# Kernel optimization log

Measured on AMD Instinct MI355X. Metric: run time of the kernel, lower is better.

The kernel has to match this reference:

```python
import jax, jax.numpy as jnp
import numpy as np

N, E, D = 40000, 320000, 128          # nodes, edges, model dim
H, C = 4, 128                          # GAT heads, per-head channels
DEPTH, MLP = 2, 512
NEG_SLOPE = 0.2
EPS_SM = 1e-16                         # PyG softmax denom epsilon


def layer_norm(x, g, b):
    mu = jnp.mean(x, axis=-1, keepdims=True)
    var = jnp.var(x, axis=-1, keepdims=True)
    return (x - mu) * jax.lax.rsqrt(var + 1e-5) * g + b


def gat_conv(x, src, dst, edge_attr, W, a_src, a_dst, We, a_edge, bias):
    # x: [N,D]; W: [D,H*C]; a_*: [H,C]; We: [1,H*C]; bias: [H*C]
    h = (x @ W).reshape(N, H, C)                       # [N,H,C]
    alpha_src = jnp.einsum('nhc,hc->nh', h, a_src)      # [N,H]
    alpha_dst = jnp.einsum('nhc,hc->nh', h, a_dst)      # [N,H]
    e = (edge_attr @ We).reshape(E, H, C)               # [E,H,C]
    alpha_e = jnp.einsum('ehc,hc->eh', e, a_edge)       # [E,H]
    alpha = alpha_src[src] + alpha_dst[dst] + alpha_e   # [E,H]
    alpha = jax.nn.leaky_relu(alpha, NEG_SLOPE)
    # segment softmax over edges sharing the same destination node
    amax = jax.ops.segment_max(alpha, dst, num_segments=N)   # [N,H]
    ex = jnp.exp(alpha - amax[dst])                          # [E,H]
    denom = jax.ops.segment_sum(ex, dst, num_segments=N)     # [N,H]
    attn = ex / (denom[dst] + EPS_SM)                        # [E,H]
    # message = attn * x_j ; aggregate by destination (scatter-add)
    msg = attn[:, :, None] * h[src]                          # [E,H,C]
    out = jax.ops.segment_sum(msg, dst, num_segments=N)      # [N,H,C]
    return out.reshape(N, H * C) + bias                      # concat heads


def setup_inputs():
    key = jax.random.key(0)
    ks = jax.random.split(key, 16)
    s = 0.05
    f32 = jnp.float32
    inp = {
        'x': jax.random.normal(ks[0], (N, D), f32),
        'edge_index': jax.random.randint(ks[1], (2, E), 0, N),
        'edge_attr': jax.random.normal(ks[2], (E, 1), f32),
        'ln1_g': jnp.ones((DEPTH, D), f32),
        'ln1_b': jnp.zeros((DEPTH, D), f32),
        'gat_W': jax.random.normal(ks[3], (DEPTH, D, H * C), f32) * s,
        'att_src': jax.random.normal(ks[4], (DEPTH, H, C), f32) * s,
        'att_dst': jax.random.normal(ks[5], (DEPTH, H, C), f32) * s,
        'edge_W': jax.random.normal(ks[6], (DEPTH, 1, H * C), f32) * s,
        'att_edge': jax.random.normal(ks[7], (DEPTH, H, C), f32) * s,
        'gat_bias': jnp.zeros((DEPTH, H * C), f32),
        'qf_W': jax.random.normal(ks[8], (DEPTH, H * C, D), f32) * s,
        'qf_b': jnp.zeros((DEPTH, D), f32),
        'ln2_g': jnp.ones((DEPTH, D), f32),
        'ln2_b': jnp.zeros((DEPTH, D), f32),
        'ff_W1': jax.random.normal(ks[9], (DEPTH, D, MLP), f32) * s,
        'ff_b1': jnp.zeros((DEPTH, MLP), f32),
        'ff_W2': jax.random.normal(ks[10], (DEPTH, MLP, D), f32) * s,
        'ff_b2': jnp.zeros((DEPTH, D), f32),
    }
    return inp


def reference(x, edge_index, edge_attr, ln1_g, ln1_b, gat_W, att_src, att_dst,
              edge_W, att_edge, gat_bias, qf_W, qf_b, ln2_g, ln2_b,
              ff_W1, ff_b1, ff_W2, ff_b2):
    src, dst = edge_index[0], edge_index[1]
    for d in range(DEPTH):
        # Residual(PreNorm(QuickFix(GATConv)))
        h = layer_norm(x, ln1_g[d], ln1_b[d])
        g = gat_conv(h, src, dst, edge_attr, gat_W[d], att_src[d], att_dst[d],
                     edge_W[d], att_edge[d], gat_bias[d])
        x = x + g @ qf_W[d] + qf_b[d]
        # Residual(PreNorm(FeedForward))
        h = layer_norm(x, ln2_g[d], ln2_b[d])
        x = x + jax.nn.gelu(h @ ff_W1[d] + ff_b1[d]) @ ff_W2[d] + ff_b2[d]
    return x
```

## Files before the change

kernel.cpp:

```cpp
#include <hip/hip_runtime.h>
#include <hip/hip_bf16.h>

#define N_NODES 40000
#define M_PAD   40064
#define N_EDGES 320000
#define DIM 128
#define HC 512
#define NHEAD 4
#define CHEAD 128
#define DEPTH_L 2
#define MLP_DIM 512
#define SCAN_NB ((N_NODES + 255) / 256)

typedef __attribute__((ext_vector_type(8))) short short8;
typedef __attribute__((ext_vector_type(4))) float f32x4;

static __device__ __forceinline__ void gload_lds16(const void* g, void* l)
{
    __builtin_amdgcn_global_load_lds(
        (const __attribute__((address_space(1))) unsigned int*)g,
        (__attribute__((address_space(3))) unsigned int*)l,
        16, 0, 0);
}

static __device__ __forceinline__ unsigned int packbf2(float a, float b)
{
    union { __hip_bfloat16 h[2]; unsigned int u; } p;
    p.h[0] = __float2bfloat16(a);
    p.h[1] = __float2bfloat16(b);
    return p.u;
}

static __device__ __forceinline__ float gelu_f(float v)
{
    float z2 = -1.5957691216f * (v + 0.044715f * v * v * v);
    return v / (1.f + __expf(z2));
}

__global__ __launch_bounds__(256) void k_ln(const float* __restrict__ x,
                                            const float* __restrict__ gma,
                                            const float* __restrict__ bta,
                                            __hip_bfloat16* __restrict__ out, int M)
{
    int row = blockIdx.x * 4 + (threadIdx.x >> 6);
    int lane = threadIdx.x & 63;
    if (row >= M) return;
    float2 v = *reinterpret_cast<const float2*>(x + (size_t)row * DIM + lane * 2);
    float s = v.x + v.y, sq = v.x * v.x + v.y * v.y;
    #pragma unroll
    for (int d = 32; d; d >>= 1) { s += __shfl_xor(s, d); sq += __shfl_xor(sq, d); }
    float mean = s * (1.f / DIM);
    float var = sq * (1.f / DIM) - mean * mean;
    float rs = rsqrtf(var + 1e-5f);
    int c = lane * 2;
    union { __hip_bfloat16 b[2]; unsigned int u; } p;
    p.b[0] = __float2bfloat16((v.x - mean) * rs * gma[c] + bta[c]);
    p.b[1] = __float2bfloat16((v.y - mean) * rs * gma[c + 1] + bta[c + 1]);
    *reinterpret_cast<unsigned int*>(out + (size_t)row * DIM + c) = p.u;
}

struct WcvtArgs {
    const float* src[4];
    __hip_bfloat16* dst[4];
    int K[4];
    int Nn[4];
};
__global__ __launch_bounds__(256) void k_wcvt4(WcvtArgs a)
{
    int j = blockIdx.y;
    int i = blockIdx.x * 256 + threadIdx.x;
    int K = a.K[j], N = a.Nn[j];
    if (i < K * N) {
        int n = i / K, k = i % K;
        a.dst[j][i] = __float2bfloat16(a.src[j][(size_t)k * N + n]);
    }
}

__global__ void k_prep_u(const float* __restrict__ gat_W,
                         const float* __restrict__ att_src,
                         const float* __restrict__ att_dst,
                         float* __restrict__ uvec)
{
    int b = blockIdx.x;
    int d = b >> 3, t8 = b & 7;
    int t = t8 >> 2, h = t8 & 3;
    int c = threadIdx.x;
    const float* W = gat_W + (size_t)d * DIM * HC;
    const float* av = (t == 0 ? att_src : att_dst) + (size_t)d * NHEAD * CHEAD + h * CHEAD;
    float s = 0.f;
    for (int cc = 0; cc < CHEAD; ++cc)
        s += W[(size_t)c * HC + h * CHEAD + cc] * av[cc];
    uvec[(size_t)d * 1024 + t8 * 128 + c] = s;
}

__global__ __launch_bounds__(256) void k_prep_m(const float* __restrict__ gat_W,
                                                const float* __restrict__ qf_W,
                                                __hip_bfloat16* __restrict__ Mt)
{
    int i = blockIdx.x * 256 + threadIdx.x;
    int d = i >> 16;
    int hk = (i >> 7) & 511;
    int j = i & 127;
    int h = hk >> 7, k = hk & 127;
    const float* W = gat_W + (size_t)d * DIM * HC + (size_t)k * HC + h * CHEAD;
    const float* Q = qf_W + (size_t)d * HC * DIM + (size_t)h * CHEAD * DIM + j;
    float s = 0.f;
    for (int c = 0; c < CHEAD; ++c)
        s += W[c] * Q[(size_t)c * DIM];
    Mt[(size_t)d * 65536 + (size_t)j * 512 + hk] = __float2bfloat16(s);
}

__global__ __launch_bounds__(256) void k_prep_c(const float* __restrict__ gat_bias,
                                                const float* __restrict__ qf_W,
                                                const float* __restrict__ qf_b,
                                                float* __restrict__ cvec)
{
    int idx = blockIdx.x * 4 + (threadIdx.x >> 6);
    int lane = threadIdx.x & 63;
    int d = idx >> 7, j = idx & 127;
    float s = 0.f;
    for (int m = lane; m < HC; m += 64)
        s += gat_bias[(size_t)d * HC + m] * qf_W[(size_t)d * HC * DIM + (size_t)m * DIM + j];
    #pragma unroll
    for (int dd = 32; dd; dd >>= 1) s += __shfl_xor(s, dd);
    if (lane == 0) cvec[idx] = s + qf_b[(size_t)d * DIM + j];
}

__global__ void k_ae(const float* __restrict__ We, const float* __restrict__ a_edge,
                     float* __restrict__ ae)
{
    int d = blockIdx.x;
    int h = threadIdx.x >> 6, lane = threadIdx.x & 63;
    float2 w = *reinterpret_cast<const float2*>(We + (size_t)d * HC + h * CHEAD + lane * 2);
    float2 a = *reinterpret_cast<const float2*>(a_edge + (size_t)d * NHEAD * CHEAD + h * CHEAD + lane * 2);
    float s = w.x * a.x + w.y * a.y;
    #pragma unroll
    for (int dd = 32; dd; dd >>= 1) s += __shfl_xor(s, dd);
    if (lane == 0) ae[d * 4 + h] = s;
}

__global__ __launch_bounds__(256) void k_dots(const unsigned int* __restrict__ hln,
                                              const float* __restrict__ uvec,
                                              float* __restrict__ asrc,
                                              float* __restrict__ adst)
{
    int n = blockIdx.x * 4 + (threadIdx.x >> 6);
    int lane = threadIdx.x & 63;
    unsigned int u = hln[n * 64 + lane];
    float f0 = __uint_as_float(u << 16);
    float f1 = __uint_as_float(u & 0xffff0000u);
    float s[8];
    #pragma unroll
    for (int t = 0; t < 8; ++t) {
        float2 uv = *reinterpret_cast<const float2*>(uvec + t * 128 + lane * 2);
        s[t] = f0 * uv.x + f1 * uv.y;
    }
    #pragma unroll
    for (int d = 32; d; d >>= 1) {
        #pragma unroll
        for (int t = 0; t < 8; ++t) s[t] += __shfl_xor(s[t], d);
    }
    if (lane == 0) {
        reinterpret_cast<float4*>(asrc)[n] = make_float4(s[0], s[1], s[2], s[3]);
        reinterpret_cast<float4*>(adst)[n] = make_float4(s[4], s[5], s[6], s[7]);
    }
}

__global__ __launch_bounds__(256) void k_alpha(const int* __restrict__ scsr,
                                               const int* __restrict__ dcsr,
                                               const float* __restrict__ eacsr,
                                               const float* __restrict__ asrc,
                                               const float* __restrict__ adst,
                                               const float* __restrict__ ae4v,
                                               float* __restrict__ wcsr)
{
    int p = blockIdx.x * 256 + threadIdx.x;
    if (p >= N_EDGES) return;
    int s = scsr[p], dd = dcsr[p];
    float q = eacsr[p];
    float4 as = reinterpret_cast<const float4*>(asrc)[s];
    float4 ad = reinterpret_cast<const float4*>(adst)[dd];
    float4 ae = *reinterpret_cast<const float4*>(ae4v);
    float4 w;
    float al;
    al = as.x + ad.x + ae.x * q; al = al > 0.f ? al : 0.2f * al; w.x = __expf(al);
    al = as.y + ad.y + ae.y * q; al = al > 0.f ? al : 0.2f * al; w.y = __expf(al);
    al = as.z + ad.z + ae.z * q; al = al > 0.f ? al : 0.2f * al; w.z = __expf(al);
    al = as.w + ad.w + ae.w * q; al = al > 0.f ? al : 0.2f * al; w.w = __expf(al);
    reinterpret_cast<float4*>(wcsr)[p] = w;
}

__global__ __launch_bounds__(256) void k_agg2(const int* __restrict__ off,
                                              const int* __restrict__ scsr,
                                              const float* __restrict__ wcsr,
                                              const unsigned int* __restrict__ hln,
                                              unsigned int* __restrict__ agg)
{
    int n = blockIdx.x * 4 + (threadIdx.x >> 6);
    int lane = threadIdx.x & 63;
    int e0 = off[n], e1 = off[n + 1];
    float den[4] = {0, 0, 0, 0};
    float accA[4] = {0, 0, 0, 0};
    float accB[4] = {0, 0, 0, 0};
    int i = e0;
    for (; i + 1 < e1; i += 2) {
        int s0 = scsr[i], s1 = scsr[i + 1];
        float4 w0 = reinterpret_cast<const float4*>(wcsr)[i];
        float4 w1 = reinterpret_cast<const float4*>(wcsr)[i + 1];
        unsigned int u0 = hln[s0 * 64 + lane];
        unsigned int u1 = hln[s1 * 64 + lane];
        float f00 = __uint_as_float(u0 << 16);
        float f01 = __uint_as_float(u0 & 0xffff0000u);
        float f10 = __uint_as_float(u1 << 16);
        float f11 = __uint_as_float(u1 & 0xffff0000u);
        den[0] += w0.x + w1.x; den[1] += w0.y + w1.y;
        den[2] += w0.z + w1.z; den[3] += w0.w + w1.w;
        accA[0] += w0.x * f00 + w1.x * f10; accB[0] += w0.x * f01 + w1.x * f11;
        accA[1] += w0.y * f00 + w1.y * f10; accB[1] += w0.y * f01 + w1.y * f11;
        accA[2] += w0.z * f00 + w1.z * f10; accB[2] += w0.z * f01 + w1.z * f11;
        accA[3] += w0.w * f00 + w1.w * f10; accB[3] += w0.w * f01 + w1.w * f11;
    }
    if (i < e1) {
        int s0 = scsr[i];
        float4 w0 = reinterpret_cast<const float4*>(wcsr)[i];
        unsigned int u0 = hln[s0 * 64 + lane];
        float f00 = __uint_as_float(u0 << 16);
        float f01 = __uint_as_float(u0 & 0xffff0000u);
        den[0] += w0.x; den[1] += w0.y; den[2] += w0.z; den[3] += w0.w;
        accA[0] += w0.x * f00; accB[0] += w0.x * f01;
        accA[1] += w0.y * f00; accB[1] += w0.y * f01;
        accA[2] += w0.z * f00; accB[2] += w0.z * f01;
        accA[3] += w0.w * f00; accB[3] += w0.w * f01;
    }
    #pragma unroll
    for (int h = 0; h < 4; ++h) {
        float inv = 1.f / (den[h] + 1e-16f);
        agg[n * 256 + h * 64 + lane] = packbf2(accA[h] * inv, accB[h] * inv);
    }
}

template <bool LN>
__global__ __launch_bounds__(256) void k_qf(const short* __restrict__ A,
                                            const short* __restrict__ Bt,
                                            const float* __restrict__ bias,
                                            const float* __restrict__ resid,
                                            float* __restrict__ xout,
                                            const float* __restrict__ gma,
                                            const float* __restrict__ bta,
                                            __hip_bfloat16* __restrict__ hout,
                                            int M)
{
    __shared__ __align__(16) short Bls[2][128 * 64];
    const int tid = threadIdx.x;
    const int lane = tid & 63;
    const int w = tid >> 6;
    const int lrow = lane & 15;
    const int lk = lane >> 4;
    const int mw = blockIdx.x * 64 + w * 16;

    auto stage = [&](int buf, int kt) {
        #pragma unroll
        for (int c0 = 0; c0 < 1024; c0 += 256) {
            int c = c0 + tid;
            int wb = c0 + (w << 6);
            int r = c >> 3, gq = c & 7, gp = gq ^ (r & 7);
            gload_lds16(Bt + (size_t)r * 512 + kt + gp * 8, &Bls[buf][wb * 8]);
        }
    };

    f32x4 acc[8] = {};
    stage(0, 0);
    __syncthreads();
    int cur = 0;
    for (int t = 0; t < 8; ++t) {
        if (t < 7) stage(cur ^ 1, (t + 1) * 64);
        #pragma unroll
        for (int ks = 0; ks < 2; ++ks) {
            short8 af = *reinterpret_cast<const short8*>(
                A + (size_t)(mw + lrow) * 512 + t * 64 + ks * 32 + lk * 8);
            short8 bf[8];
            #pragma unroll
            for (int fj = 0; fj < 8; ++fj) {
                int r = fj * 16 + lrow;
                int g = ks * 4 + lk;
                bf[fj] = *reinterpret_cast<const short8*>(
                    &Bls[cur][r * 64 + ((g ^ (r & 7)) * 8)]);
            }
            #pragma unroll
            for (int fj = 0; fj < 8; ++fj)
                acc[fj] = __builtin_amdgcn_mfma_f32_16x16x32_bf16(
                    af, bf[fj], acc[fj], 0, 0, 0);
        }
        __syncthreads();
        cur ^= 1;
    }

    #pragma unroll
    for (int p = 0; p < 4; ++p) {
        int m = mw + lk * 4 + p;
        float v[8], s = 0.f, sq = 0.f;
        #pragma unroll
        for (int fj = 0; fj < 8; ++fj) {
            int n = fj * 16 + lrow;
            v[fj] = acc[fj][p] + bias[n] + resid[(size_t)m * DIM + n];
            s += v[fj]; sq += v[fj] * v[fj];
        }
        #pragma unroll
        for (int fj = 0; fj < 8; ++fj)
            xout[(size_t)m * DIM + fj * 16 + lrow] = v[fj];
        if (LN) {
            #pragma unroll
            for (int d = 1; d < 16; d <<= 1) {
                s += __shfl_xor(s, d);
                sq += __shfl_xor(sq, d);
            }
            float mean = s * (1.f / DIM);
            float var = sq * (1.f / DIM) - mean * mean;
            float rs = rsqrtf(var + 1e-5f);
            #pragma unroll
            for (int fj = 0; fj < 8; ++fj) {
                int n = fj * 16 + lrow;
                hout[(size_t)m * DIM + n] =
                    __float2bfloat16((v[fj] - mean) * rs * gma[n] + bta[n]);
            }
        }
    }
}

template <bool LN>
__global__ __launch_bounds__(256) void k_ff(const short* __restrict__ A,
                                            const short* __restrict__ W1t,
                                            const short* __restrict__ W2t,
                                            const float* __restrict__ b1,
                                            const float* __restrict__ b2,
                                            const float* __restrict__ resid,
                                            float* __restrict__ xout,
                                            const float* __restrict__ gma,
                                            const float* __restrict__ bta,
                                            __hip_bfloat16* __restrict__ hout,
                                            int M)
{
    __shared__ __align__(16) short B1ls[64 * 128];
    __shared__ __align__(16) short B2ls[128 * 64];
    __shared__ __align__(16) short midls[4][16 * 64];
    const int tid = threadIdx.x;
    const int lane = tid & 63;
    const int w = tid >> 6;
    const int lrow = lane & 15;
    const int lk = lane >> 4;
    const int mw = blockIdx.x * 64 + w * 16;
    __hip_bfloat16* midw = (__hip_bfloat16*)midls[w];

    short8 af[4];
    #pragma unroll
    for (int ks = 0; ks < 4; ++ks)
        af[ks] = *reinterpret_cast<const short8*>(
            A + (size_t)(mw + lrow) * 128 + ks * 32 + lk * 8);

    auto stage1 = [&](int mc) {
        #pragma unroll
        for (int c0 = 0; c0 < 1024; c0 += 256) {
            int c = c0 + tid;
            int wb = c0 + (w << 6);
            int r = c >> 4, gq = c & 15, gp = gq ^ (r & 15);
            gload_lds16(W1t + (size_t)(mc * 64 + r) * 128 + gp * 8, &B1ls[wb * 8]);
        }
    };
    auto stage2 = [&](int mc) {
        #pragma unroll
        for (int c0 = 0; c0 < 1024; c0 += 256) {
            int c = c0 + tid;
            int wb = c0 + (w << 6);
            int r = c >> 3, gq = c & 7, gp = gq ^ (r & 7);
            gload_lds16(W2t + (size_t)r * 512 + mc * 64 + gp * 8, &B2ls[wb * 8]);
        }
    };

    f32x4 acc2[8] = {};
    stage1(0);
    for (int mc = 0; mc < 8; ++mc) {
        __syncthreads();
        stage2(mc);
        f32x4 acc1[4] = {};
        #pragma unroll
        for (int ks = 0; ks < 4; ++ks) {
            short8 bf1[4];
            #pragma unroll
            for (int fj = 0; fj < 4; ++fj) {
                int r = fj * 16 + lrow;
                bf1[fj] = *reinterpret_cast<const short8*>(
                    &B1ls[r * 128 + (((ks * 4 + lk) ^ (r & 15)) * 8)]);
            }
            #pragma unroll
            for (int fj = 0; fj < 4; ++fj)
                acc1[fj] = __builtin_amdgcn_mfma_f32_16x16x32_bf16(
                    af[ks], bf1[fj], acc1[fj], 0, 0, 0);
        }
        #pragma unroll
        for (int fj = 0; fj < 4; ++fj) {
            #pragma unroll
            for (int p = 0; p < 4; ++p) {
                int mloc = lk * 4 + p;
                int cloc = fj * 16 + lrow;
                float v = gelu_f(acc1[fj][p] + b1[mc * 64 + cloc]);
                int slot = (cloc >> 3) ^ (mloc & 7);
                midw[mloc * 64 + slot * 8 + (cloc & 7)] = __float2bfloat16(v);
            }
        }
        __syncthreads();
        if (mc < 7) stage1(mc + 1);
        #pragma unroll
        for (int ks2 = 0; ks2 < 2; ++ks2) {
            int g = ks2 * 4 + lk;
            short8 a2 = *reinterpret_cast<const short8*>(
                &midls[w][lrow * 64 + ((g ^ (lrow & 7)) * 8)]);
            short8 bf2[8];
            #pragma unroll
            for (int fj = 0; fj < 8; ++fj) {
                int r = fj * 16 + lrow;
                bf2[fj] = *reinterpret_cast<const short8*>(
                    &B2ls[r * 64 + (((g ^ (r & 7))) * 8)]);
            }
            #pragma unroll
            for (int fj = 0; fj < 8; ++fj)
                acc2[fj] = __builtin_amdgcn_mfma_f32_16x16x32_bf16(
                    a2, bf2[fj], acc2[fj], 0, 0, 0);
        }
    }

    #pragma unroll
    for (int p = 0; p < 4; ++p) {
        int m = mw + lk * 4 + p;
        float v[8], s = 0.f, sq = 0.f;
        #pragma unroll
        for (int fj = 0; fj < 8; ++fj) {
            int n = fj * 16 + lrow;
            v[fj] = acc2[fj][p] + b2[n] + resid[(size_t)m * DIM + n];
            s += v[fj]; sq += v[fj] * v[fj];
        }
        #pragma unroll
        for (int fj = 0; fj < 8; ++fj)
            xout[(size_t)m * DIM + fj * 16 + lrow] = v[fj];
        if (LN) {
            #pragma unroll
            for (int d = 1; d < 16; d <<= 1) {
                s += __shfl_xor(s, d);
                sq += __shfl_xor(sq, d);
            }
            float mean = s * (1.f / DIM);
            float var = sq * (1.f / DIM) - mean * mean;
            float rs = rsqrtf(var + 1e-5f);
            #pragma unroll
            for (int fj = 0; fj < 8; ++fj) {
                int n = fj * 16 + lrow;
                hout[(size_t)m * DIM + n] =
                    __float2bfloat16((v[fj] - mean) * rs * gma[n] + bta[n]);
            }
        }
    }
}

__global__ void k_hist(const int* __restrict__ dst, int* __restrict__ deg)
{
    int e = blockIdx.x * 256 + threadIdx.x;
    if (e < N_EDGES) atomicAdd(&deg[dst[e]], 1);
}

__global__ __launch_bounds__(256) void k_scan1(const int* __restrict__ deg,
                                               int* __restrict__ off,
                                               int* __restrict__ bsum)
{
    __shared__ int wsum[4];
    int b = blockIdx.x;
    int t = threadIdx.x, lane = t & 63, w = t >> 6;
    int i = b * 256 + t;
    int v = (i < N_NODES) ? deg[i] : 0;
    int s = v;
    #pragma unroll
    for (int d = 1; d < 64; d <<= 1) {
        int u = __shfl_up(s, d);
        if (lane >= d) s += u;
    }
    if (lane == 63) wsum[w] = s;
    __syncthreads();
    int wpre = 0;
    #pragma unroll
    for (int j = 0; j < 4; ++j)
        if (j < w) wpre += wsum[j];
    if (i < N_NODES) off[i] = wpre + s - v;
    if (t == 255) bsum[b] = wpre + s;
}

__global__ __launch_bounds__(256) void k_scan2(int* __restrict__ bsum,
                                               int* __restrict__ bpre)
{
    __shared__ int wsum[4];
    int t = threadIdx.x, lane = t & 63, w = t >> 6;
    int v = (t < SCAN_NB) ? bsum[t] : 0;
    int s = v;
    #pragma unroll
    for (int d = 1; d < 64; d <<= 1) {
        int u = __shfl_up(s, d);
        if (lane >= d) s += u;
    }
    if (lane == 63) wsum[w] = s;
    __syncthreads();
    int wpre = 0;
    #pragma unroll
    for (int j = 0; j < 4; ++j)
        if (j < w) wpre += wsum[j];
    if (t < SCAN_NB) bpre[t] = wpre + s - v;
    if (t == 255) bpre[SCAN_NB] = wpre + s;
}

__global__ __launch_bounds__(256) void k_scan3(int* __restrict__ off,
                                               const int* __restrict__ bpre,
                                               int* __restrict__ cur)
{
    int b = blockIdx.x;
    int i = b * 256 + threadIdx.x;
    if (i < N_NODES) {
        int o = off[i] + bpre[b];
        off[i] = o;
        cur[i] = o;
    }
    if (i == 0) off[N_NODES] = bpre[SCAN_NB];
}

__global__ void k_fill(const int* __restrict__ src, const int* __restrict__ dst,
                       const float* __restrict__ ea, int* __restrict__ cur,
                       int* __restrict__ scsr, int* __restrict__ dcsr,
                       float* __restrict__ eacsr)
{
    int e = blockIdx.x * 256 + threadIdx.x;
    if (e < N_EDGES) {
        int dd = dst[e];
        int p = atomicAdd(&cur[dd], 1);
        scsr[p] = src[e];
        dcsr[p] = dd;
        eacsr[p] = ea[e];
    }
}

extern "C" void kernel_launch(void* const* d_in, const int* in_sizes, int n_in,
                              void* d_out, int out_size, void* d_ws, size_t ws_size,
                              hipStream_t stream)
{
    const float* x_in     = (const float*)d_in[0];
    const int*   ei       = (const int*)d_in[1];
    const float* ea       = (const float*)d_in[2];
    const float* ln1_g    = (const float*)d_in[3];
    const float* ln1_b    = (const float*)d_in[4];
    const float* gat_W    = (const float*)d_in[5];
    const float* att_src  = (const float*)d_in[6];
    const float* att_dst  = (const float*)d_in[7];
    const float* edge_W   = (const float*)d_in[8];
    const float* att_edge = (const float*)d_in[9];
    const float* gat_bias = (const float*)d_in[10];
    const float* qf_W     = (const float*)d_in[11];
    const float* qf_b     = (const float*)d_in[12];
    const float* ln2_g    = (const float*)d_in[13];
    const float* ln2_b    = (const float*)d_in[14];
    const float* ff_W1    = (const float*)d_in[15];
    const float* ff_b1    = (const float*)d_in[16];
    const float* ff_W2    = (const float*)d_in[17];
    const float* ff_b2    = (const float*)d_in[18];
    float* x = (float*)d_out;

    char* ws = (char*)d_ws;
    size_t o = 0;
    auto alloc = [&](size_t b) { size_t r = o; o += (b + 255) & ~(size_t)255; return r; };
    __hip_bfloat16*  h_ln  = (__hip_bfloat16*)(ws + alloc((size_t)M_PAD * DIM * 2));
    __hip_bfloat16*  gbuf  = (__hip_bfloat16*)(ws + alloc((size_t)M_PAD * HC * 2));
    float*           asrc  = (float*)(ws + alloc((size_t)N_NODES * 4 * 4));
    float*           adst  = (float*)(ws + alloc((size_t)N_NODES * 4 * 4));
    float*           ae4   = (float*)(ws + alloc(256));
    float*           uvec  = (float*)(ws + alloc((size_t)DEPTH_L * 1024 * 4));
    __hip_bfloat16*  Mt    = (__hip_bfloat16*)(ws + alloc((size_t)DEPTH_L * 65536 * 2));
    float*           cvec  = (float*)(ws + alloc(256 * 4));
    int*             deg   = (int*)(ws + alloc((size_t)(N_NODES + 1) * 4));
    int*             off   = (int*)(ws + alloc((size_t)(N_NODES + 1) * 4));
    int*             cur   = (int*)(ws + alloc((size_t)N_NODES * 4));
    int*             bsum  = (int*)(ws + alloc((size_t)(SCAN_NB + 1) * 4));
    int*             bpre  = (int*)(ws + alloc((size_t)(SCAN_NB + 1) * 4));
    int*             scsr  = (int*)(ws + alloc((size_t)N_EDGES * 4));
    int*             dcsr  = (int*)(ws + alloc((size_t)N_EDGES * 4));
    float*           eacsr = (float*)(ws + alloc((size_t)N_EDGES * 4));
    float*           wcsr  = (float*)(ws + alloc((size_t)N_EDGES * 4 * 4));
    __hip_bfloat16* Wt[DEPTH_L][2];
    for (int d = 0; d < DEPTH_L; ++d)
        for (int j = 0; j < 2; ++j)
            Wt[d][j] = (__hip_bfloat16*)(ws + alloc((size_t)65536 * 2));

    const int* srcA = ei;
    const int* dstA = ei + N_EDGES;

    WcvtArgs wa;
    for (int d = 0; d < DEPTH_L; ++d) {
        wa.src[d * 2 + 0] = ff_W1 + (size_t)d * DIM * MLP_DIM; wa.K[d * 2 + 0] = DIM;     wa.Nn[d * 2 + 0] = MLP_DIM;
        wa.src[d * 2 + 1] = ff_W2 + (size_t)d * MLP_DIM * DIM; wa.K[d * 2 + 1] = MLP_DIM; wa.Nn[d * 2 + 1] = DIM;
        wa.dst[d * 2 + 0] = Wt[d][0];
        wa.dst[d * 2 + 1] = Wt[d][1];
    }
    k_wcvt4<<<dim3(256, 4), 256, 0, stream>>>(wa);
    k_prep_u<<<16, 128, 0, stream>>>(gat_W, att_src, att_dst, uvec);
    k_prep_m<<<512, 256, 0, stream>>>(gat_W, qf_W, Mt);
    k_prep_c<<<64, 256, 0, stream>>>(gat_bias, qf_W, qf_b, cvec);
    k_ae<<<2, 256, 0, stream>>>(edge_W, att_edge, ae4);

    hipMemsetAsync(deg, 0, (size_t)(N_NODES + 1) * 4, stream);
    k_hist<<<(N_EDGES + 255) / 256, 256, 0, stream>>>(dstA, deg);
    k_scan1<<<SCAN_NB, 256, 0, stream>>>(deg, off, bsum);
    k_scan2<<<1, 256, 0, stream>>>(bsum, bpre);
    k_scan3<<<SCAN_NB, 256, 0, stream>>>(off, bpre, cur);
    k_fill<<<(N_EDGES + 255) / 256, 256, 0, stream>>>(srcA, dstA, ea, cur, scsr, dcsr, eacsr);

    const int QB = N_NODES / 64;
    const int NB = N_NODES / 4;
    const int EB = (N_EDGES + 255) / 256;

    k_ln<<<NB, 256, 0, stream>>>(x_in, ln1_g, ln1_b, h_ln, N_NODES);
    k_dots<<<NB, 256, 0, stream>>>((const unsigned int*)h_ln, uvec, asrc, adst);

    for (int d = 0; d < DEPTH_L; ++d) {
        const float* resid0 = (d == 0) ? x_in : x;
        k_alpha<<<EB, 256, 0, stream>>>(scsr, dcsr, eacsr, asrc, adst, ae4 + d * 4, wcsr);
        k_agg2<<<NB, 256, 0, stream>>>(off, scsr, wcsr, (const unsigned int*)h_ln,
            (unsigned int*)gbuf);
        k_qf<true><<<QB, 256, 0, stream>>>((const short*)gbuf,
            (const short*)(Mt + (size_t)d * 65536), cvec + d * 128, resid0, x,
            ln2_g + d * DIM, ln2_b + d * DIM, h_ln, N_NODES);
        if (d + 1 < DEPTH_L) {
            k_ff<true><<<QB, 256, 0, stream>>>((const short*)h_ln,
                (const short*)Wt[d][0], (const short*)Wt[d][1],
                ff_b1 + d * MLP_DIM, ff_b2 + d * DIM, x, x,
                ln1_g + (d + 1) * DIM, ln1_b + (d + 1) * DIM, h_ln, N_NODES);
            k_dots<<<NB, 256, 0, stream>>>((const unsigned int*)h_ln,
                uvec + (size_t)(d + 1) * 1024, asrc, adst);
        } else {
            k_ff<false><<<QB, 256, 0, stream>>>((const short*)h_ln,
                (const short*)Wt[d][0], (const short*)Wt[d][1],
                ff_b1 + d * MLP_DIM, ff_b2 + d * DIM, x, x,
                nullptr, nullptr, nullptr, N_NODES);
        }
    }
}
```

Measured before the change: 295.9 us.

## Merge prep kernels, build CSR in one grid-barrier kernel, fuse LN with dots

Folds the five weight-preprocessing kernels into one block-indexed k_prep launch. Replaces the memset, histogram, three scan kernels and fill with a single persistent k_csr kernel that separates its phases with atomic-counter grid barriers. Fuses the first LayerNorm with the attention-score dot products, and preloads all A fragments into registers in k_qf. The goal is fewer launches and less intermediate traffic; the cost is reliance on all 512 CSR blocks being co-resident for the spin barrier, plus higher register pressure in k_qf.

```diff
diff --git a/kernel.cpp b/kernel.cpp
--- a/kernel.cpp
+++ b/kernel.cpp
@@ -2,7 +2,6 @@
 #include <hip/hip_bf16.h>
 
 #define N_NODES 40000
-#define M_PAD   40064
 #define N_EDGES 320000
 #define DIM 128
 #define HC 512
@@ -11,6 +10,7 @@
 #define DEPTH_L 2
 #define MLP_DIM 512
 #define SCAN_NB ((N_NODES + 255) / 256)
+#define CSR_NB 512
 
 typedef __attribute__((ext_vector_type(8))) short short8;
 typedef __attribute__((ext_vector_type(4))) float f32x4;
@@ -37,10 +37,185 @@
     return v / (1.f + __expf(z2));
 }
 
+struct PrepArgs {
+    const float* wsrc[4];
+    __hip_bfloat16* wdst[4];
+    int wK[4];
+    int wN[4];
+    const float* gat_W;
+    const float* att_src;
+    const float* att_dst;
+    const float* edge_W;
+    const float* att_edge;
+    const float* gat_bias;
+    const float* qf_W;
+    const float* qf_b;
+    float* uvec;
+    __hip_bfloat16* Mt;
+    float* cvec;
+    float* ae;
+    int* cnt;
+};
+__global__ __launch_bounds__(256) void k_prep(PrepArgs a)
+{
+    int b = blockIdx.x;
+    int tid = threadIdx.x;
+    if (b < 1024) {
+        int j = b >> 8;
+        int i = (b & 255) * 256 + tid;
+        int K = a.wK[j], N = a.wN[j];
+        if (i < K * N) {
+            int n = i / K, k = i % K;
+            a.wdst[j][i] = __float2bfloat16(a.wsrc[j][(size_t)k * N + n]);
+        }
+    } else if (b < 1040) {
+        if (tid < 128) {
+            int bb = b - 1024;
+            int d = bb >> 3, t8 = bb & 7;
+            int t = t8 >> 2, h = t8 & 3;
+            int c = tid;
+            const float* W = a.gat_W + (size_t)d * DIM * HC;
+            const float* av = (t == 0 ? a.att_src : a.att_dst)
+                              + (size_t)d * NHEAD * CHEAD + h * CHEAD;
+            float s = 0.f;
+            for (int cc = 0; cc < CHEAD; ++cc)
+                s += W[(size_t)c * HC + h * CHEAD + cc] * av[cc];
+            a.uvec[(size_t)d * 1024 + t8 * 128 + c] = s;
+        }
+    } else if (b < 1552) {
+        int i = (b - 1040) * 256 + tid;
+        int d = i >> 16;
+        int hk = (i >> 7) & 511;
+        int j = i & 127;
+        int h = hk >> 7, k = hk & 127;
+        const float* W = a.gat_W + (size_t)d * DIM * HC + (size_t)k * HC + h * CHEAD;
+        const float* Q = a.qf_W + (size_t)d * HC * DIM + (size_t)h * CHEAD * DIM + j;
+        float s = 0.f;
+        for (int c = 0; c < CHEAD; ++c)
+            s += W[c] * Q[(size_t)c * DIM];
+        a.Mt[(size_t)d * 65536 + (size_t)j * 512 + hk] = __float2bfloat16(s);
+    } else if (b < 1616) {
+        int idx = (b - 1552) * 4 + (tid >> 6);
+        int lane = tid & 63;
+        int d = idx >> 7, j = idx & 127;
+        float s = 0.f;
+        for (int m = lane; m < HC; m += 64)
+            s += a.gat_bias[(size_t)d * HC + m]
+               * a.qf_W[(size_t)d * HC * DIM + (size_t)m * DIM + j];
+        #pragma unroll
+        for (int dd = 32; dd; dd >>= 1) s += __shfl_xor(s, dd);
+        if (lane == 0) a.cvec[idx] = s + a.qf_b[(size_t)d * DIM + j];
+    } else if (b < 1618) {
+        int d = b - 1616;
+        int h = tid >> 6, lane = tid & 63;
+        float2 w = *reinterpret_cast<const float2*>(
+            a.edge_W + (size_t)d * HC + h * CHEAD + lane * 2);
+        float2 av = *reinterpret_cast<const float2*>(
+            a.att_edge + (size_t)d * NHEAD * CHEAD + h * CHEAD + lane * 2);
+        float s = w.x * av.x + w.y * av.y;
+        #pragma unroll
+        for (int dd = 32; dd; dd >>= 1) s += __shfl_xor(s, dd);
+        if (lane == 0) a.ae[d * 4 + h] = s;
+    } else {
+        if (tid < 8) a.cnt[tid] = 0;
+    }
+}
+
+static __device__ __forceinline__ void gbar(int* cnt, int phase)
+{
+    __syncthreads();
+    if (threadIdx.x == 0) {
+        __threadfence();
+        atomicAdd(&cnt[phase], 1);
+        while (atomicAdd(&cnt[phase], 0) < CSR_NB) __builtin_amdgcn_s_sleep(8);
+        __threadfence();
+    }
+    __syncthreads();
+}
+
+__global__ __launch_bounds__(256) void k_csr(const int* __restrict__ src,
+                                             const int* __restrict__ dst,
+                                             const float* __restrict__ ea,
+                                             int* __restrict__ deg,
+                                             int* __restrict__ off,
+                                             int* __restrict__ cur,
+                                             int* __restrict__ bsum,
+                                             int* __restrict__ bpre,
+                                             int* __restrict__ scsr,
+                                             int* __restrict__ dcsr,
+                                             float* __restrict__ eacsr,
+                                             int* cnt)
+{
+    __shared__ int wsum[4];
+    int t = threadIdx.x, lane = t & 63, w = t >> 6;
+    int gtid = blockIdx.x * 256 + t;
+    const int gsz = CSR_NB * 256;
+
+    for (int i = gtid; i <= N_NODES; i += gsz) deg[i] = 0;
+    gbar(cnt, 0);
+    for (int e = gtid; e < N_EDGES; e += gsz) atomicAdd(&deg[dst[e]], 1);
+    gbar(cnt, 1);
+    for (int b = blockIdx.x; b < SCAN_NB; b += CSR_NB) {
+        int i = b * 256 + t;
+        int v = (i < N_NODES) ? deg[i] : 0;
+        int s = v;
+        #pragma unroll
+        for (int d = 1; d < 64; d <<= 1) {
+            int u = __shfl_up(s, d);
+            if (lane >= d) s += u;
+        }
+        if (lane == 63) wsum[w] = s;
+        __syncthreads();
+        int wpre = 0;
+        #pragma unroll
+        for (int j = 0; j < 4; ++j)
+            if (j < w) wpre += wsum[j];
+        if (i < N_NODES) off[i] = wpre + s - v;
+        if (t == 255) bsum[b] = wpre + s;
+        __syncthreads();
+    }
+    gbar(cnt, 2);
+    if (blockIdx.x == 0) {
+        int v = (t < SCAN_NB) ? bsum[t] : 0;
+        int s = v;
+        #pragma unroll
+        for (int d = 1; d < 64; d <<= 1) {
+            int u = __shfl_up(s, d);
+            if (lane >= d) s += u;
+        }
+        if (lane == 63) wsum[w] = s;
+        __syncthreads();
+        int wpre = 0;
+        #pragma unroll
+        for (int j = 0; j < 4; ++j)
+            if (j < w) wpre += wsum[j];
+        if (t < SCAN_NB) bpre[t] = wpre + s - v;
+        if (t == 255) bpre[SCAN_NB] = wpre + s;
+    }
+    gbar(cnt, 3);
+    for (int i = gtid; i < N_NODES; i += gsz) {
+        int o = off[i] + bpre[i >> 8];
+        off[i] = o;
+        cur[i] = o;
+    }
+    if (gtid == 0) off[N_NODES] = bpre[SCAN_NB];
+    gbar(cnt, 4);
+    for (int e = gtid; e < N_EDGES; e += gsz) {
+        int dd = dst[e];
+        int p = atomicAdd(&cur[dd], 1);
+        scsr[p] = src[e];
+        dcsr[p] = dd;
+        eacsr[p] = ea[e];
+    }
+}
+
 __global__ __launch_bounds__(256) void k_ln(const float* __restrict__ x,
                                             const float* __restrict__ gma,
                                             const float* __restrict__ bta,
-                                            __hip_bfloat16* __restrict__ out, int M)
+                                            const float* __restrict__ uvec,
+                                            __hip_bfloat16* __restrict__ out,
+                                            float* __restrict__ asrc,
+                                            float* __restrict__ adst, int M)
 {
     int row = blockIdx.x * 4 + (threadIdx.x >> 6);
     int lane = threadIdx.x & 63;
@@ -53,90 +228,24 @@
     float var = sq * (1.f / DIM) - mean * mean;
     float rs = rsqrtf(var + 1e-5f);
     int c = lane * 2;
-    union { __hip_bfloat16 b[2]; unsigned int u; } p;
-    p.b[0] = __float2bfloat16((v.x - mean) * rs * gma[c] + bta[c]);
-    p.b[1] = __float2bfloat16((v.y - mean) * rs * gma[c + 1] + bta[c + 1]);
-    *reinterpret_cast<unsigned int*>(out + (size_t)row * DIM + c) = p.u;
-}
-
-struct WcvtArgs {
-    const float* src[4];
-    __hip_bfloat16* dst[4];
-    int K[4];
-    int Nn[4];
-};
-__global__ __launch_bounds__(256) void k_wcvt4(WcvtArgs a)
-{
-    int j = blockIdx.y;
-    int i = blockIdx.x * 256 + threadIdx.x;
-    int K = a.K[j], N = a.Nn[j];
-    if (i < K * N) {
-        int n = i / K, k = i % K;
-        a.dst[j][i] = __float2bfloat16(a.src[j][(size_t)k * N + n]);
-    }
-}
-
-__global__ void k_prep_u(const float* __restrict__ gat_W,
-                         const float* __restrict__ att_src,
-                         const float* __restrict__ att_dst,
-                         float* __restrict__ uvec)
-{
-    int b = blockIdx.x;
-    int d = b >> 3, t8 = b & 7;
-    int t = t8 >> 2, h = t8 & 3;
-    int c = threadIdx.x;
-    const float* W = gat_W + (size_t)d * DIM * HC;
-    const float* av = (t == 0 ? att_src : att_dst) + (size_t)d * NHEAD * CHEAD + h * CHEAD;
-    float s = 0.f;
-    for (int cc = 0; cc < CHEAD; ++cc)
-        s += W[(size_t)c * HC + h * CHEAD + cc] * av[cc];
-    uvec[(size_t)d * 1024 + t8 * 128 + c] = s;
-}
-
-__global__ __launch_bounds__(256) void k_prep_m(const float* __restrict__ gat_W,
-                                                const float* __restrict__ qf_W,
-                                                __hip_bfloat16* __restrict__ Mt)
-{
-    int i = blockIdx.x * 256 + threadIdx.x;
-    int d = i >> 16;
-    int hk = (i >> 7) & 511;
-    int j = i & 127;
-    int h = hk >> 7, k = hk & 127;
-    const float* W = gat_W + (size_t)d * DIM * HC + (size_t)k * HC + h * CHEAD;
-    const float* Q = qf_W + (size_t)d * HC * DIM + (size_t)h * CHEAD * DIM + j;
-    float s = 0.f;
-    for (int c = 0; c < CHEAD; ++c)
-        s += W[c] * Q[(size_t)c * DIM];
-    Mt[(size_t)d * 65536 + (size_t)j * 512 + hk] = __float2bfloat16(s);
-}
-
-__global__ __launch_bounds__(256) void k_prep_c(const float* __restrict__ gat_bias,
-                                                const float* __restrict__ qf_W,
-                                                const float* __restrict__ qf_b,
-                                                float* __restrict__ cvec)
-{
-    int idx = blockIdx.x * 4 + (threadIdx.x >> 6);
-    int lane = threadIdx.x & 63;
-    int d = idx >> 7, j = idx & 127;
-    float s = 0.f;
-    for (int m = lane; m < HC; m += 64)
-        s += gat_bias[(size_t)d * HC + m] * qf_W[(size_t)d * HC * DIM + (size_t)m * DIM + j];
-    #pragma unroll
-    for (int dd = 32; dd; dd >>= 1) s += __shfl_xor(s, dd);
-    if (lane == 0) cvec[idx] = s + qf_b[(size_t)d * DIM + j];
-}
-
-__global__ void k_ae(const float* __restrict__ We, const float* __restrict__ a_edge,
-                     float* __restrict__ ae)
-{
-    int d = blockIdx.x;
-    int h = threadIdx.x >> 6, lane = threadIdx.x & 63;
-    float2 w = *reinterpret_cast<const float2*>(We + (size_t)d * HC + h * CHEAD + lane * 2);
-    float2 a = *reinterpret_cast<const float2*>(a_edge + (size_t)d * NHEAD * CHEAD + h * CHEAD + lane * 2);
-    float s = w.x * a.x + w.y * a.y;
-    #pragma unroll
-    for (int dd = 32; dd; dd >>= 1) s += __shfl_xor(s, dd);
-    if (lane == 0) ae[d * 4 + h] = s;
+    float h0 = (v.x - mean) * rs * gma[c] + bta[c];
+    float h1 = (v.y - mean) * rs * gma[c + 1] + bta[c + 1];
+    *reinterpret_cast<unsigned int*>(out + (size_t)row * DIM + c) = packbf2(h0, h1);
+    float ss[8];
+    #pragma unroll
+    for (int tt = 0; tt < 8; ++tt) {
+        float2 uv = *reinterpret_cast<const float2*>(uvec + tt * 128 + c);
+        ss[tt] = h0 * uv.x + h1 * uv.y;
+    }
+    #pragma unroll
+    for (int d = 32; d; d >>= 1) {
+        #pragma unroll
+        for (int tt = 0; tt < 8; ++tt) ss[tt] += __shfl_xor(ss[tt], d);
+    }
+    if (lane == 0) {
+        reinterpret_cast<float4*>(asrc)[row] = make_float4(ss[0], ss[1], ss[2], ss[3]);
+        reinterpret_cast<float4*>(adst)[row] = make_float4(ss[4], ss[5], ss[6], ss[7]);
+    }
 }
 
 __global__ __launch_bounds__(256) void k_dots(const unsigned int* __restrict__ hln,
@@ -258,6 +367,12 @@
     const int lk = lane >> 4;
     const int mw = blockIdx.x * 64 + w * 16;
 
+    short8 aq[16];
+    #pragma unroll
+    for (int t = 0; t < 16; ++t)
+        aq[t] = *reinterpret_cast<const short8*>(
+            A + (size_t)(mw + lrow) * 512 + t * 32 + lk * 8);
+
     auto stage = [&](int buf, int kt) {
         #pragma unroll
         for (int c0 = 0; c0 < 1024; c0 += 256) {
@@ -276,8 +391,7 @@
         if (t < 7) stage(cur ^ 1, (t + 1) * 64);
         #pragma unroll
         for (int ks = 0; ks < 2; ++ks) {
-            short8 af = *reinterpret_cast<const short8*>(
-                A + (size_t)(mw + lrow) * 512 + t * 64 + ks * 32 + lk * 8);
+            short8 af = aq[t * 2 + ks];
             short8 bf[8];
             #pragma unroll
             for (int fj = 0; fj < 8; ++fj) {
@@ -327,7 +441,7 @@
     }
 }
 
-template <bool LN>
+template <bool LNN>
 __global__ __launch_bounds__(256) void k_ff(const short* __restrict__ A,
                                             const short* __restrict__ W1t,
                                             const short* __restrict__ W2t,
@@ -419,7 +533,7 @@
             for (int fj = 0; fj < 8; ++fj) {
                 int r = fj * 16 + lrow;
                 bf2[fj] = *reinterpret_cast<const short8*>(
-                    &B2ls[r * 64 + (((g ^ (r & 7))) * 8)]);
+                    &B2ls[r * 64 + ((g ^ (r & 7)) * 8)]);
             }
             #pragma unroll
             for (int fj = 0; fj < 8; ++fj)
@@ -441,7 +555,7 @@
         #pragma unroll
         for (int fj = 0; fj < 8; ++fj)
             xout[(size_t)m * DIM + fj * 16 + lrow] = v[fj];
-        if (LN) {
+        if (LNN) {
             #pragma unroll
             for (int d = 1; d < 16; d <<= 1) {
                 s += __shfl_xor(s, d);
@@ -457,88 +571,6 @@
                     __float2bfloat16((v[fj] - mean) * rs * gma[n] + bta[n]);
             }
         }
-    }
-}
-
-__global__ void k_hist(const int* __restrict__ dst, int* __restrict__ deg)
-{
-    int e = blockIdx.x * 256 + threadIdx.x;
-    if (e < N_EDGES) atomicAdd(&deg[dst[e]], 1);
-}
-
-__global__ __launch_bounds__(256) void k_scan1(const int* __restrict__ deg,
-                                               int* __restrict__ off,
-                                               int* __restrict__ bsum)
-{
-    __shared__ int wsum[4];
-    int b = blockIdx.x;
-    int t = threadIdx.x, lane = t & 63, w = t >> 6;
-    int i = b * 256 + t;
-    int v = (i < N_NODES) ? deg[i] : 0;
-    int s = v;
-    #pragma unroll
-    for (int d = 1; d < 64; d <<= 1) {
-        int u = __shfl_up(s, d);
-        if (lane >= d) s += u;
-    }
-    if (lane == 63) wsum[w] = s;
-    __syncthreads();
-    int wpre = 0;
-    #pragma unroll
-    for (int j = 0; j < 4; ++j)
-        if (j < w) wpre += wsum[j];
-    if (i < N_NODES) off[i] = wpre + s - v;
-    if (t == 255) bsum[b] = wpre + s;
-}
-
-__global__ __launch_bounds__(256) void k_scan2(int* __restrict__ bsum,
-                                               int* __restrict__ bpre)
-{
-    __shared__ int wsum[4];
-    int t = threadIdx.x, lane = t & 63, w = t >> 6;
-    int v = (t < SCAN_NB) ? bsum[t] : 0;
-    int s = v;
-    #pragma unroll
-    for (int d = 1; d < 64; d <<= 1) {
-        int u = __shfl_up(s, d);
-        if (lane >= d) s += u;
-    }
-    if (lane == 63) wsum[w] = s;
-    __syncthreads();
-    int wpre = 0;
-    #pragma unroll
-    for (int j = 0; j < 4; ++j)
-        if (j < w) wpre += wsum[j];
-    if (t < SCAN_NB) bpre[t] = wpre + s - v;
-    if (t == 255) bpre[SCAN_NB] = wpre + s;
-}
-
-__global__ __launch_bounds__(256) void k_scan3(int* __restrict__ off,
-                                               const int* __restrict__ bpre,
-                                               int* __restrict__ cur)
-{
-    int b = blockIdx.x;
-    int i = b * 256 + threadIdx.x;
-    if (i < N_NODES) {
-        int o = off[i] + bpre[b];
-        off[i] = o;
-        cur[i] = o;
-    }
-    if (i == 0) off[N_NODES] = bpre[SCAN_NB];
-}
-
-__global__ void k_fill(const int* __restrict__ src, const int* __restrict__ dst,
-                       const float* __restrict__ ea, int* __restrict__ cur,
-                       int* __restrict__ scsr, int* __restrict__ dcsr,
-                       float* __restrict__ eacsr)
-{
-    int e = blockIdx.x * 256 + threadIdx.x;
-    if (e < N_EDGES) {
-        int dd = dst[e];
-        int p = atomicAdd(&cur[dd], 1);
-        scsr[p] = src[e];
-        dcsr[p] = dd;
-        eacsr[p] = ea[e];
     }
 }
 
@@ -570,14 +602,15 @@
     char* ws = (char*)d_ws;
     size_t o = 0;
     auto alloc = [&](size_t b) { size_t r = o; o += (b + 255) & ~(size_t)255; return r; };
-    __hip_bfloat16*  h_ln  = (__hip_bfloat16*)(ws + alloc((size_t)M_PAD * DIM * 2));
-    __hip_bfloat16*  gbuf  = (__hip_bfloat16*)(ws + alloc((size_t)M_PAD * HC * 2));
+    __hip_bfloat16*  h_ln  = (__hip_bfloat16*)(ws + alloc((size_t)N_NODES * DIM * 2));
+    __hip_bfloat16*  gbuf  = (__hip_bfloat16*)(ws + alloc((size_t)N_NODES * HC * 2));
     float*           asrc  = (float*)(ws + alloc((size_t)N_NODES * 4 * 4));
     float*           adst  = (float*)(ws + alloc((size_t)N_NODES * 4 * 4));
     float*           ae4   = (float*)(ws + alloc(256));
     float*           uvec  = (float*)(ws + alloc((size_t)DEPTH_L * 1024 * 4));
     __hip_bfloat16*  Mt    = (__hip_bfloat16*)(ws + alloc((size_t)DEPTH_L * 65536 * 2));
     float*           cvec  = (float*)(ws + alloc(256 * 4));
+    int*             cnt   = (int*)(ws + alloc(64));
     int*             deg   = (int*)(ws + alloc((size_t)(N_NODES + 1) * 4));
     int*             off   = (int*)(ws + alloc((size_t)(N_NODES + 1) * 4));
     int*             cur   = (int*)(ws + alloc((size_t)N_NODES * 4));
@@ -595,32 +628,29 @@
     const int* srcA = ei;
     const int* dstA = ei + N_EDGES;
 
-    WcvtArgs wa;
+    PrepArgs pa;
     for (int d = 0; d < DEPTH_L; ++d) {
-        wa.src[d * 2 + 0] = ff_W1 + (size_t)d * DIM * MLP_DIM; wa.K[d * 2 + 0] = DIM;     wa.Nn[d * 2 + 0] = MLP_DIM;
-        wa.src[d * 2 + 1] = ff_W2 + (size_t)d * MLP_DIM * DIM; wa.K[d * 2 + 1] = MLP_DIM; wa.Nn[d * 2 + 1] = DIM;
-        wa.dst[d * 2 + 0] = Wt[d][0];
-        wa.dst[d * 2 + 1] = Wt[d][1];
-    }
-    k_wcvt4<<<dim3(256, 4), 256, 0, stream>>>(wa);
-    k_prep_u<<<16, 128, 0, stream>>>(gat_W, att_src, att_dst, uvec);
-    k_prep_m<<<512, 256, 0, stream>>>(gat_W, qf_W, Mt);
-    k_prep_c<<<64, 256, 0, stream>>>(gat_bias, qf_W, qf_b, cvec);
-    k_ae<<<2, 256, 0, stream>>>(edge_W, att_edge, ae4);
-
-    hipMemsetAsync(deg, 0, (size_t)(N_NODES + 1) * 4, stream);
-    k_hist<<<(N_EDGES + 255) / 256, 256, 0, stream>>>(dstA, deg);
-    k_scan1<<<SCAN_NB, 256, 0, stream>>>(deg, off, bsum);
-    k_scan2<<<1, 256, 0, stream>>>(bsum, bpre);
-    k_scan3<<<SCAN_NB, 256, 0, stream>>>(off, bpre, cur);
-    k_fill<<<(N_EDGES + 255) / 256, 256, 0, stream>>>(srcA, dstA, ea, cur, scsr, dcsr, eacsr);
+        pa.wsrc[d * 2 + 0] = ff_W1 + (size_t)d * DIM * MLP_DIM;
+        pa.wK[d * 2 + 0] = DIM;     pa.wN[d * 2 + 0] = MLP_DIM;
+        pa.wsrc[d * 2 + 1] = ff_W2 + (size_t)d * MLP_DIM * DIM;
+        pa.wK[d * 2 + 1] = MLP_DIM; pa.wN[d * 2 + 1] = DIM;
+        pa.wdst[d * 2 + 0] = Wt[d][0];
+        pa.wdst[d * 2 + 1] = Wt[d][1];
+    }
+    pa.gat_W = gat_W; pa.att_src = att_src; pa.att_dst = att_dst;
+    pa.edge_W = edge_W; pa.att_edge = att_edge;
+    pa.gat_bias = gat_bias; pa.qf_W = qf_W; pa.qf_b = qf_b;
+    pa.uvec = uvec; pa.Mt = Mt; pa.cvec = cvec; pa.ae = ae4; pa.cnt = cnt;
+    k_prep<<<1619, 256, 0, stream>>>(pa);
+
+    k_csr<<<CSR_NB, 256, 0, stream>>>(srcA, dstA, ea, deg, off, cur, bsum, bpre,
+                                      scsr, dcsr, eacsr, cnt);
 
     const int QB = N_NODES / 64;
     const int NB = N_NODES / 4;
     const int EB = (N_EDGES + 255) / 256;
 
-    k_ln<<<NB, 256, 0, stream>>>(x_in, ln1_g, ln1_b, h_ln, N_NODES);
-    k_dots<<<NB, 256, 0, stream>>>((const unsigned int*)h_ln, uvec, asrc, adst);
+    k_ln<<<NB, 256, 0, stream>>>(x_in, ln1_g, ln1_b, uvec, h_ln, asrc, adst, N_NODES);
 
     for (int d = 0; d < DEPTH_L; ++d) {
         const float* resid0 = (d == 0) ? x_in : x;
```

New measurement: 461.8 us. 56.1% more time.
